# Kernel optimization log

Measured on AMD Instinct MI355X. Metric: run time of the kernel, lower is better.

The kernel has to match this reference:

```python
import jax, jax.numpy as jnp
import numpy as np

N_ANCHORS = 10647
N_CLASSES = 80
N_OUT = 5 + N_CLASSES
N_GT = 2048
POS_IOU = 0.7
NEG_IOU = 0.3
N_SAMPLE = 256
POS_RATIO = 0.5


def _cxcy_to_corners(b):
    return jnp.concatenate([b[:, :2] - b[:, 2:4] / 2, b[:, :2] + b[:, 2:4] / 2], axis=-1)


def _iou(a, b):
    # a: [N,4] corner boxes, b: [M,4] corner boxes -> [N,M]
    lt = jnp.maximum(a[:, None, :2], b[None, :, :2])
    rb = jnp.minimum(a[:, None, 2:], b[None, :, 2:])
    wh = jnp.clip(rb - lt, 0.0)
    inter = wh[..., 0] * wh[..., 1]
    area_a = (a[:, 2] - a[:, 0]) * (a[:, 3] - a[:, 1])
    area_b = (b[:, 2] - b[:, 0]) * (b[:, 3] - b[:, 1])
    return inter / (area_a[:, None] + area_b[None, :] - inter)


def _bce_logits(x, t):
    # numerically stable BCEWithLogits, elementwise
    return jnp.maximum(x, 0.0) - x * t + jnp.log1p(jnp.exp(-jnp.abs(x)))


def _demote_first(labels, value, excess):
    # demote the first `excess` anchors (in index order) whose label == value to -1,
    # mirroring torch's nonzero()[randperm(excess)] which always hits the first
    # `excess` entries of the nonzero list
    m = labels == value
    cum = jnp.cumsum(m.astype(jnp.int32))
    return jnp.where(m & (cum <= excess), -1.0, labels)


def _generate_targets(priors, gt_boxes, gt_labels):
    ious = _iou(_cxcy_to_corners(priors[:, :4]), _cxcy_to_corners(gt_boxes))  # [N, M]
    gt_max_index = jnp.argmax(ious, axis=0)       # [M] best anchor per gt
    anchor_max_ious = jnp.max(ious, axis=1)       # [N]
    anchor_max_index = jnp.argmax(ious, axis=1)   # [N]
    labels = jnp.full((N_ANCHORS,), -1.0, dtype=ious.dtype)
    labels = labels.at[gt_max_index].set(1.0)
    labels = jnp.where(anchor_max_ious >= POS_IOU, 1.0, labels)
    labels = jnp.where(anchor_max_ious < NEG_IOU, 0.0, labels)
    n_pos_quota = int(POS_RATIO * N_SAMPLE)
    n_pos_actual = jnp.sum(labels == 1.0)
    labels = _demote_first(labels, 1.0, jnp.maximum(n_pos_actual - n_pos_quota, 0))
    n_neg_req = N_SAMPLE - jnp.sum(labels == 1.0)
    n_neg_actual = jnp.sum(labels == 0.0)
    labels = _demote_first(labels, 0.0, jnp.maximum(n_neg_actual - n_neg_req, 0))
    anchor_gt_box = gt_boxes[anchor_max_index]    # [N,4] matched gt box per anchor
    anchor_cls = gt_labels[anchor_max_index] + 5  # [N] one-hot class column per anchor
    targets = jnp.zeros((N_ANCHORS, N_OUT), dtype=gt_boxes.dtype)
    targets = targets.at[:, :4].set(anchor_gt_box)
    targets = targets.at[:, 4].set(labels)
    targets = targets.at[jnp.arange(N_ANCHORS), anchor_cls].set(1.0)
    return targets


def _forward(predictions, gt_boxes, gt_labels, priors):
    targets = _generate_targets(priors, gt_boxes, gt_labels)
    pred = predictions[0]                          # [N, N_OUT]
    labels = targets[:, 4]
    pos = (labels == 1.0).astype(pred.dtype)
    neg = (labels == 0.0).astype(pred.dtype)
    n_pos = jnp.maximum(jnp.sum(pos), 1.0)
    n_neg = jnp.maximum(jnp.sum(neg), 1.0)
    # masked-mean MSE over x,y,w,h on positive anchors
    diff2 = (pred[:, :4] - targets[:, :4]) ** 2
    loss_box = jnp.sum(pos[:, None] * diff2, axis=0) / n_pos
    loss_conf_obj = jnp.sum(pos * _bce_logits(pred[:, 4], targets[:, 4])) / n_pos
    loss_conf_nonobj = jnp.sum(neg * _bce_logits(pred[:, 4], targets[:, 4])) / n_neg
    loss_class = jnp.sum(pos[:, None] * _bce_logits(pred[:, 5:], targets[:, 5:])) / (n_pos * N_CLASSES)
    total_loss = jnp.sum(loss_box) + loss_conf_obj + loss_conf_nonobj + loss_class
    return pred, total_loss


def setup_inputs() -> dict:
    key = jax.random.key(0)
    k1, k2, k3, k4 = jax.random.split(key, 4)
    predictions = jax.random.normal(k1, (1, N_ANCHORS, N_OUT), dtype=jnp.float32)
    gt_boxes = jax.random.uniform(k2, (N_GT, 4), dtype=jnp.float32, minval=0.05, maxval=0.95)
    gt_labels = jax.random.randint(k3, (N_GT,), 0, N_CLASSES)
    priors = jax.random.uniform(k4, (N_ANCHORS, N_OUT), dtype=jnp.float32, minval=0.05, maxval=0.95)
    return {"predictions": predictions, "gt_boxes": gt_boxes, "gt_labels": gt_labels, "priors": priors}


def reference(predictions, gt_boxes, gt_labels, priors):
    return _forward(predictions, gt_boxes, gt_labels, priors)
```

## Files before the change

kernel.cpp:

```cpp
#include <hip/hip_runtime.h>
#include <math.h>

#define N_ANCH 10647
#define NA_PAD 10688
#define N_GT   2048
#define N_OUTC 85
#define PRED_ELEMS (N_ANCH * N_OUTC)
#define PRED_V4    (PRED_ELEMS / 4)
#define N_CHUNK    42

#define ABX 21
#define ABY 32
#define NBLK_A (ABX * ABY)
#define GBX 4
#define GBY 167
#define NBLK_G (GBX * GBY)
#define NBLK_IOU (NBLK_A + NBLK_G)
#define CPY_PER_BLK ((PRED_V4 + NBLK_IOU - 1) / NBLK_IOU)

struct WS {
    float4 ac[NA_PAD];
    float4 gc[N_GT];
    unsigned long long akey[N_ANCH];
    unsigned long long gkey[N_GT];
    float aa[NA_PAD];
    float ga[N_GT];
    int cnt_p[N_CHUNK], cnt_n[N_CHUNK];
    unsigned int sync;
};

__device__ __forceinline__ float bce(float x, float t) {
    return fmaxf(x, 0.0f) - x * t + log1pf(expf(-fabsf(x)));
}

__device__ __forceinline__ unsigned long long packkey(float iou, int idx) {
    return ((unsigned long long)__float_as_uint(iou) << 32) |
           (unsigned)(~(unsigned)idx);
}

__global__ __launch_bounds__(256) void k_prep(const float* __restrict__ gtb,
                                              const float* __restrict__ priors,
                                              WS* __restrict__ ws) {
    int i = blockIdx.x * 256 + threadIdx.x;
    if (i < NA_PAD) {
        float4 c = make_float4(0.f, 0.f, 0.f, 0.f);
        float ar = 0.f;
        if (i < N_ANCH) {
            float cx = priors[i*N_OUTC+0], cy = priors[i*N_OUTC+1];
            float w  = priors[i*N_OUTC+2], h  = priors[i*N_OUTC+3];
            c = make_float4(cx - w*0.5f, cy - h*0.5f, cx + w*0.5f, cy + h*0.5f);
            ar = (c.z - c.x) * (c.w - c.y);
            ws->akey[i] = 0ull;
        }
        ws->ac[i] = c;
        ws->aa[i] = ar;
    }
    if (i < N_GT) {
        float4 v = ((const float4*)gtb)[i];
        float4 c = make_float4(v.x - v.z*0.5f, v.y - v.w*0.5f,
                               v.x + v.z*0.5f, v.y + v.w*0.5f);
        ws->gc[i] = c;
        ws->ga[i] = (c.z - c.x) * (c.w - c.y);
        ws->gkey[i] = 0ull;
    }
    if (i == 0) ws->sync = 0u;
}

__global__ __launch_bounds__(256) void k_iou(const float* __restrict__ pred,
                                             float* __restrict__ out,
                                             WS* __restrict__ ws) {
    int b = blockIdx.x, t = threadIdx.x;
    if (t < CPY_PER_BLK) {
        int idx = b * CPY_PER_BLK + t;
        if (idx < PRED_V4)
            ((float4*)out)[idx] = ((const float4*)pred)[idx];
    }
    if (b == 0 && t == 0) {
        out[PRED_ELEMS - 3] = pred[PRED_ELEMS - 3];
        out[PRED_ELEMS - 2] = pred[PRED_ELEMS - 2];
        out[PRED_ELEMS - 1] = pred[PRED_ELEMS - 1];
        out[PRED_ELEMS] = 0.0f;
    }

    if (b < NBLK_A) {
        int bx = b % ABX, by = b / ABX;
        int jbase = by * 64;
        int i0 = bx * 512 + t, i1 = i0 + 256;
        bool v0 = (i0 < N_ANCH), v1 = (i1 < N_ANCH);
        int ri0 = v0 ? i0 : 0, ri1 = v1 ? i1 : 0;
        float4 a0 = ws->ac[ri0]; float aa0 = ws->aa[ri0];
        float4 a1 = ws->ac[ri1]; float aa1 = ws->aa[ri1];
        float I0 = -1.f, S0 = 1.f, I1 = -1.f, S1 = 1.f;
        int bj0 = 0, bj1 = 0;
#pragma unroll 4
        for (int jj = 0; jj < 64; ++jj) {
            float4 g = ws->gc[jbase + jj];
            float ga = ws->ga[jbase + jj];
            float lx = fmaxf(a0.x, g.x), ly = fmaxf(a0.y, g.y);
            float rx = fminf(a0.z, g.z), ry = fminf(a0.w, g.w);
            float In = fmaxf(rx - lx, 0.f) * fmaxf(ry - ly, 0.f);
            float Sn = aa0 + ga;
            bool c = In * S0 > I0 * Sn;
            I0 = c ? In : I0; S0 = c ? Sn : S0; bj0 = c ? jj : bj0;
            lx = fmaxf(a1.x, g.x); ly = fmaxf(a1.y, g.y);
            rx = fminf(a1.z, g.z); ry = fminf(a1.w, g.w);
            In = fmaxf(rx - lx, 0.f) * fmaxf(ry - ly, 0.f);
            Sn = aa1 + ga;
            c = In * S1 > I1 * Sn;
            I1 = c ? In : I1; S1 = c ? Sn : S1; bj1 = c ? jj : bj1;
        }
        if (v0) atomicMax(&ws->akey[i0], packkey(I0 / (S0 - I0), jbase + bj0));
        if (v1) atomicMax(&ws->akey[i1], packkey(I1 / (S1 - I1), jbase + bj1));
    } else {
        int b2 = b - NBLK_A;
        int bx = b2 % GBX, by = b2 / GBX;
        int ibase = by * 64;
        int j0 = bx * 512 + t, j1 = j0 + 256;
        float4 g0 = ws->gc[j0]; float ga0 = ws->ga[j0];
        float4 g1 = ws->gc[j1]; float ga1 = ws->ga[j1];
        float I0 = -1.f, S0 = 1.f, I1 = -1.f, S1 = 1.f;
        int bi0 = 0, bi1 = 0;
#pragma unroll 4
        for (int ii = 0; ii < 64; ++ii) {
            float4 a = ws->ac[ibase + ii];
            float aa = ws->aa[ibase + ii];
            float lx = fmaxf(a.x, g0.x), ly = fmaxf(a.y, g0.y);
            float rx = fminf(a.z, g0.z), ry = fminf(a.w, g0.w);
            float In = fmaxf(rx - lx, 0.f) * fmaxf(ry - ly, 0.f);
            float Sn = aa + ga0;
            bool c = In * S0 > I0 * Sn;
            I0 = c ? In : I0; S0 = c ? Sn : S0; bi0 = c ? ii : bi0;
            lx = fmaxf(a.x, g1.x); ly = fmaxf(a.y, g1.y);
            rx = fminf(a.z, g1.z); ry = fminf(a.w, g1.w);
            In = fmaxf(rx - lx, 0.f) * fmaxf(ry - ly, 0.f);
            Sn = aa + ga1;
            c = In * S1 > I1 * Sn;
            I1 = c ? In : I1; S1 = c ? Sn : S1; bi1 = c ? ii : bi1;
        }
        atomicMax(&ws->gkey[j0], packkey(I0 / (S0 - I0), ibase + bi0));
        atomicMax(&ws->gkey[j1], packkey(I1 / (S1 - I1), ibase + bi1));
    }
}

__global__ __launch_bounds__(256) void k_tail2(const float* __restrict__ pred,
                                               const float* __restrict__ gtb,
                                               const int* __restrict__ gtl,
                                               WS* __restrict__ ws,
                                               float* __restrict__ out) {
    __shared__ int sFlg[256];
    __shared__ int wA[4], wB[4];
    __shared__ int wps[4], wns[4];
    __shared__ int sCp[N_CHUNK], sCn[N_CHUNK];
    __shared__ int    sPosI[256];
    __shared__ float4 sPosBox[256];
    __shared__ int    sPosCls[256];
    __shared__ int    sNegI[256];
    __shared__ float  red[12];
    int b = blockIdx.x, t = threadIdx.x, lane = t & 63, wid = t >> 6;
    int base = b * 256;

    sFlg[t] = 0;
    __syncthreads();
    for (int j = t; j < N_GT; j += 256) {
        int ai = (int)(~(unsigned)(ws->gkey[j]));
        int rel = ai - base;
        if ((unsigned)rel < 256u) sFlg[rel] = 1;
    }
    __syncthreads();
    int i = base + t;
    int lab = -2;
    if (i < N_ANCH) {
        float amax = __uint_as_float((unsigned)(ws->akey[i] >> 32));
        lab = (amax < 0.3f) ? 0 : ((amax >= 0.7f || sFlg[t]) ? 1 : -1);
    }
    bool f1 = (lab == 1), f0 = (lab == 0);
    unsigned long long b1 = __ballot(f1), b0v = __ballot(f0);
    if (lane == 0) { wA[wid] = __popcll(b1); wB[wid] = __popcll(b0v); }
    __syncthreads();
    if (t == 0) {
        int cp = wA[0] + wA[1] + wA[2] + wA[3];
        int cn = wB[0] + wB[1] + wB[2] + wB[3];
        __hip_atomic_store(&ws->cnt_p[b], cp, __ATOMIC_RELAXED, __HIP_MEMORY_SCOPE_AGENT);
        __hip_atomic_store(&ws->cnt_n[b], cn, __ATOMIC_RELAXED, __HIP_MEMORY_SCOPE_AGENT);
        __hip_atomic_fetch_add(&ws->sync, 1u, __ATOMIC_RELEASE, __HIP_MEMORY_SCOPE_AGENT);
        while (__hip_atomic_load(&ws->sync, __ATOMIC_ACQUIRE, __HIP_MEMORY_SCOPE_AGENT)
               < (unsigned)N_CHUNK)
            __builtin_amdgcn_s_sleep(2);
    }
    __syncthreads();
    if (t < N_CHUNK) {
        sCp[t] = __hip_atomic_load(&ws->cnt_p[t], __ATOMIC_ACQUIRE, __HIP_MEMORY_SCOPE_AGENT);
        sCn[t] = __hip_atomic_load(&ws->cnt_n[t], __ATOMIC_ACQUIRE, __HIP_MEMORY_SCOPE_AGENT);
    }
    __syncthreads();
    int npa = 0, nna = 0, pb = 0, nb = 0;
#pragma unroll
    for (int c = 0; c < N_CHUNK; ++c) {
        int cp = sCp[c], cn = sCn[c];
        if (c < b) { pb += cp; nb += cn; }
        npa += cp; nna += cn;
    }
    int excess_pos = (npa > 128) ? (npa - 128) : 0;
    int n_pos_f = npa - excess_pos;
    int n_neg_req = 256 - n_pos_f;
    int excess_neg = (nna > n_neg_req) ? (nna - n_neg_req) : 0;
    int n_neg_f = nna - excess_neg;

    unsigned long long pm = (2ull << lane) - 1ull;
    int r1 = __popcll(b1 & pm), r0 = __popcll(b0v & pm);
    if (lane == 0) { wps[wid] = __popcll(b1); wns[wid] = __popcll(b0v); }
    __syncthreads();
    int p1 = 0, p0 = 0, cpB = 0, cnB = 0;
    for (int w = 0; w < 4; ++w) {
        int v1 = wps[w], v0 = wns[w];
        cpB += v1; cnB += v0;
        if (w < wid) { p1 += v1; p0 += v0; }
    }
    int thp = excess_pos - pb; thp = (thp < 0) ? 0 : thp;
    int thn = excess_neg - nb; thn = (thn < 0) ? 0 : thn;
    if (f1) {
        int L = p1 + r1;
        if (L > thp) {
            int slot = L - thp - 1;
            sPosI[slot] = i;
            unsigned am = ~(unsigned)(ws->akey[i]);
            sPosBox[slot] = ((const float4*)gtb)[am];
            sPosCls[slot] = gtl[am] + 5;
        }
    }
    if (f0) {
        int L = p0 + r0;
        if (L > thn) sNegI[L - thn - 1] = i;
    }
    __syncthreads();
    int nP = cpB - thp; nP = (nP < 0) ? 0 : nP;
    int nN = cnB - thn; nN = (nN < 0) ? 0 : nN;

    float acc_a = 0.f, acc_c = 0.f, acc_n = 0.f;
    int nT = nP * N_OUTC;
    for (int u = t; u < nT; u += 256) {
        int pi = u / N_OUTC, col = u - pi * N_OUTC;
        float p = pred[sPosI[pi] * N_OUTC + col];
        if (col < 4) {
            float d = p - ((const float*)&sPosBox[pi])[col];
            acc_a += d * d;
        } else if (col == 4) {
            acc_a += bce(p, 1.0f);
        } else {
            acc_c += bce(p, (col == sPosCls[pi]) ? 1.0f : 0.0f);
        }
    }
    for (int u = t; u < nN; u += 256)
        acc_n += bce(pred[sNegI[u] * N_OUTC + 4], 0.0f);

    for (int o = 32; o; o >>= 1) {
        acc_a += __shfl_down(acc_a, o);
        acc_c += __shfl_down(acc_c, o);
        acc_n += __shfl_down(acc_n, o);
    }
    if (lane == 0) { red[wid] = acc_a; red[4 + wid] = acc_c; red[8 + wid] = acc_n; }
    __syncthreads();
    if (t == 0) {
        float A  = red[0] + red[1] + red[2]  + red[3];
        float C  = red[4] + red[5] + red[6]  + red[7];
        float Nn = red[8] + red[9] + red[10] + red[11];
        float np = fmaxf((float)n_pos_f, 1.0f);
        float nn = fmaxf((float)n_neg_f, 1.0f);
        float contrib = A / np + Nn / nn + C / (np * 80.0f);
        if (contrib != 0.0f) atomicAdd(&out[PRED_ELEMS], contrib);
    }
}

extern "C" void kernel_launch(void* const* d_in, const int* in_sizes, int n_in,
                              void* d_out, int out_size, void* d_ws, size_t ws_size,
                              hipStream_t stream) {
    const float* pred   = (const float*)d_in[0];
    const float* gtb    = (const float*)d_in[1];
    const int*   gtl    = (const int*)d_in[2];
    const float* priors = (const float*)d_in[3];
    float* out = (float*)d_out;
    WS* ws = (WS*)d_ws;

    k_prep<<<dim3(N_CHUNK), 256, 0, stream>>>(gtb, priors, ws);
    k_iou<<<dim3(NBLK_IOU), 256, 0, stream>>>(pred, out, ws);
    k_tail2<<<dim3(N_CHUNK), 256, 0, stream>>>(pred, gtb, gtl, ws, out);
}
```

Measured before the change: 65.98 us.

## Fuse prep, IoU and tail kernels into one persistent kernel with grid barriers

```diff
diff --git a/kernel.cpp b/kernel.cpp
--- a/kernel.cpp
+++ b/kernel.cpp
@@ -11,14 +11,17 @@
 
 #define ABX 21
 #define ABY 32
-#define NBLK_A (ABX * ABY)
+#define NTILE_A (ABX * ABY)
 #define GBX 4
 #define GBY 167
-#define NBLK_G (GBX * GBY)
-#define NBLK_IOU (NBLK_A + NBLK_G)
-#define CPY_PER_BLK ((PRED_V4 + NBLK_IOU - 1) / NBLK_IOU)
+#define NTILE (NTILE_A + GBX * GBY)
+#define NBLK 512
+#define NTHREADS (NBLK * 256)
 
 struct WS {
+    unsigned int sync_b1; unsigned int pad1[31];
+    unsigned int sync_b2; unsigned int pad2[31];
+    unsigned int sync_t;  unsigned int pad3[31];
     float4 ac[NA_PAD];
     float4 gc[N_GT];
     unsigned long long akey[N_ANCH];
@@ -26,8 +29,8 @@
     float aa[NA_PAD];
     float ga[N_GT];
     int cnt_p[N_CHUNK], cnt_n[N_CHUNK];
-    unsigned int sync;
 };
+#define MEMSET_BYTES 384
 
 __device__ __forceinline__ float bce(float x, float t) {
     return fmaxf(x, 0.0f) - x * t + log1pf(expf(-fabsf(x)));
@@ -38,115 +41,12 @@
            (unsigned)(~(unsigned)idx);
 }
 
-__global__ __launch_bounds__(256) void k_prep(const float* __restrict__ gtb,
-                                              const float* __restrict__ priors,
-                                              WS* __restrict__ ws) {
-    int i = blockIdx.x * 256 + threadIdx.x;
-    if (i < NA_PAD) {
-        float4 c = make_float4(0.f, 0.f, 0.f, 0.f);
-        float ar = 0.f;
-        if (i < N_ANCH) {
-            float cx = priors[i*N_OUTC+0], cy = priors[i*N_OUTC+1];
-            float w  = priors[i*N_OUTC+2], h  = priors[i*N_OUTC+3];
-            c = make_float4(cx - w*0.5f, cy - h*0.5f, cx + w*0.5f, cy + h*0.5f);
-            ar = (c.z - c.x) * (c.w - c.y);
-            ws->akey[i] = 0ull;
-        }
-        ws->ac[i] = c;
-        ws->aa[i] = ar;
-    }
-    if (i < N_GT) {
-        float4 v = ((const float4*)gtb)[i];
-        float4 c = make_float4(v.x - v.z*0.5f, v.y - v.w*0.5f,
-                               v.x + v.z*0.5f, v.y + v.w*0.5f);
-        ws->gc[i] = c;
-        ws->ga[i] = (c.z - c.x) * (c.w - c.y);
-        ws->gkey[i] = 0ull;
-    }
-    if (i == 0) ws->sync = 0u;
-}
-
-__global__ __launch_bounds__(256) void k_iou(const float* __restrict__ pred,
-                                             float* __restrict__ out,
-                                             WS* __restrict__ ws) {
-    int b = blockIdx.x, t = threadIdx.x;
-    if (t < CPY_PER_BLK) {
-        int idx = b * CPY_PER_BLK + t;
-        if (idx < PRED_V4)
-            ((float4*)out)[idx] = ((const float4*)pred)[idx];
-    }
-    if (b == 0 && t == 0) {
-        out[PRED_ELEMS - 3] = pred[PRED_ELEMS - 3];
-        out[PRED_ELEMS - 2] = pred[PRED_ELEMS - 2];
-        out[PRED_ELEMS - 1] = pred[PRED_ELEMS - 1];
-        out[PRED_ELEMS] = 0.0f;
-    }
-
-    if (b < NBLK_A) {
-        int bx = b % ABX, by = b / ABX;
-        int jbase = by * 64;
-        int i0 = bx * 512 + t, i1 = i0 + 256;
-        bool v0 = (i0 < N_ANCH), v1 = (i1 < N_ANCH);
-        int ri0 = v0 ? i0 : 0, ri1 = v1 ? i1 : 0;
-        float4 a0 = ws->ac[ri0]; float aa0 = ws->aa[ri0];
-        float4 a1 = ws->ac[ri1]; float aa1 = ws->aa[ri1];
-        float I0 = -1.f, S0 = 1.f, I1 = -1.f, S1 = 1.f;
-        int bj0 = 0, bj1 = 0;
-#pragma unroll 4
-        for (int jj = 0; jj < 64; ++jj) {
-            float4 g = ws->gc[jbase + jj];
-            float ga = ws->ga[jbase + jj];
-            float lx = fmaxf(a0.x, g.x), ly = fmaxf(a0.y, g.y);
-            float rx = fminf(a0.z, g.z), ry = fminf(a0.w, g.w);
-            float In = fmaxf(rx - lx, 0.f) * fmaxf(ry - ly, 0.f);
-            float Sn = aa0 + ga;
-            bool c = In * S0 > I0 * Sn;
-            I0 = c ? In : I0; S0 = c ? Sn : S0; bj0 = c ? jj : bj0;
-            lx = fmaxf(a1.x, g.x); ly = fmaxf(a1.y, g.y);
-            rx = fminf(a1.z, g.z); ry = fminf(a1.w, g.w);
-            In = fmaxf(rx - lx, 0.f) * fmaxf(ry - ly, 0.f);
-            Sn = aa1 + ga;
-            c = In * S1 > I1 * Sn;
-            I1 = c ? In : I1; S1 = c ? Sn : S1; bj1 = c ? jj : bj1;
-        }
-        if (v0) atomicMax(&ws->akey[i0], packkey(I0 / (S0 - I0), jbase + bj0));
-        if (v1) atomicMax(&ws->akey[i1], packkey(I1 / (S1 - I1), jbase + bj1));
-    } else {
-        int b2 = b - NBLK_A;
-        int bx = b2 % GBX, by = b2 / GBX;
-        int ibase = by * 64;
-        int j0 = bx * 512 + t, j1 = j0 + 256;
-        float4 g0 = ws->gc[j0]; float ga0 = ws->ga[j0];
-        float4 g1 = ws->gc[j1]; float ga1 = ws->ga[j1];
-        float I0 = -1.f, S0 = 1.f, I1 = -1.f, S1 = 1.f;
-        int bi0 = 0, bi1 = 0;
-#pragma unroll 4
-        for (int ii = 0; ii < 64; ++ii) {
-            float4 a = ws->ac[ibase + ii];
-            float aa = ws->aa[ibase + ii];
-            float lx = fmaxf(a.x, g0.x), ly = fmaxf(a.y, g0.y);
-            float rx = fminf(a.z, g0.z), ry = fminf(a.w, g0.w);
-            float In = fmaxf(rx - lx, 0.f) * fmaxf(ry - ly, 0.f);
-            float Sn = aa + ga0;
-            bool c = In * S0 > I0 * Sn;
-            I0 = c ? In : I0; S0 = c ? Sn : S0; bi0 = c ? ii : bi0;
-            lx = fmaxf(a.x, g1.x); ly = fmaxf(a.y, g1.y);
-            rx = fminf(a.z, g1.z); ry = fminf(a.w, g1.w);
-            In = fmaxf(rx - lx, 0.f) * fmaxf(ry - ly, 0.f);
-            Sn = aa + ga1;
-            c = In * S1 > I1 * Sn;
-            I1 = c ? In : I1; S1 = c ? Sn : S1; bi1 = c ? ii : bi1;
-        }
-        atomicMax(&ws->gkey[j0], packkey(I0 / (S0 - I0), ibase + bi0));
-        atomicMax(&ws->gkey[j1], packkey(I1 / (S1 - I1), ibase + bi1));
-    }
-}
-
-__global__ __launch_bounds__(256) void k_tail2(const float* __restrict__ pred,
+__global__ __launch_bounds__(256) void k_fused(const float* __restrict__ pred,
                                                const float* __restrict__ gtb,
                                                const int* __restrict__ gtl,
-                                               WS* __restrict__ ws,
-                                               float* __restrict__ out) {
+                                               const float* __restrict__ priors,
+                                               float* __restrict__ out,
+                                               WS* __restrict__ ws) {
     __shared__ int sFlg[256];
     __shared__ int wA[4], wB[4];
     __shared__ int wps[4], wns[4];
@@ -156,9 +56,123 @@
     __shared__ int    sPosCls[256];
     __shared__ int    sNegI[256];
     __shared__ float  red[12];
+
     int b = blockIdx.x, t = threadIdx.x, lane = t & 63, wid = t >> 6;
+    int gtid = b * 256 + t;
+
+    for (int idx = gtid; idx < PRED_V4; idx += NTHREADS)
+        ((float4*)out)[idx] = ((const float4*)pred)[idx];
+    if (gtid == 0) {
+        out[PRED_ELEMS - 3] = pred[PRED_ELEMS - 3];
+        out[PRED_ELEMS - 2] = pred[PRED_ELEMS - 2];
+        out[PRED_ELEMS - 1] = pred[PRED_ELEMS - 1];
+        out[PRED_ELEMS] = 0.0f;
+    }
+    if (gtid < NA_PAD) {
+        float4 c = make_float4(0.f, 0.f, 0.f, 0.f);
+        float ar = 0.f;
+        if (gtid < N_ANCH) {
+            float cx = priors[gtid*N_OUTC+0], cy = priors[gtid*N_OUTC+1];
+            float w  = priors[gtid*N_OUTC+2], h  = priors[gtid*N_OUTC+3];
+            c = make_float4(cx - w*0.5f, cy - h*0.5f, cx + w*0.5f, cy + h*0.5f);
+            ar = (c.z - c.x) * (c.w - c.y);
+            ws->akey[gtid] = 0ull;
+        }
+        ws->ac[gtid] = c;
+        ws->aa[gtid] = ar;
+    }
+    if (gtid < N_GT) {
+        float4 v = ((const float4*)gtb)[gtid];
+        float4 c = make_float4(v.x - v.z*0.5f, v.y - v.w*0.5f,
+                               v.x + v.z*0.5f, v.y + v.w*0.5f);
+        ws->gc[gtid] = c;
+        ws->ga[gtid] = (c.z - c.x) * (c.w - c.y);
+        ws->gkey[gtid] = 0ull;
+    }
+
+    __syncthreads();
+    if (t == 0) {
+        __hip_atomic_fetch_add(&ws->sync_b1, 1u, __ATOMIC_RELEASE, __HIP_MEMORY_SCOPE_AGENT);
+        while (__hip_atomic_load(&ws->sync_b1, __ATOMIC_ACQUIRE, __HIP_MEMORY_SCOPE_AGENT)
+               < (unsigned)NBLK)
+            __builtin_amdgcn_s_sleep(2);
+    }
+    __syncthreads();
+
+    for (int vb = b; vb < NTILE; vb += NBLK) {
+        if (vb < NTILE_A) {
+            int bx = vb % ABX, by = vb / ABX;
+            int jbase = by * 64;
+            int i0 = bx * 512 + t, i1 = i0 + 256;
+            bool v0 = (i0 < N_ANCH), v1 = (i1 < N_ANCH);
+            int ri0 = v0 ? i0 : 0, ri1 = v1 ? i1 : 0;
+            float4 a0 = ws->ac[ri0]; float aa0 = ws->aa[ri0];
+            float4 a1 = ws->ac[ri1]; float aa1 = ws->aa[ri1];
+            float I0 = -1.f, S0 = 1.f, I1 = -1.f, S1 = 1.f;
+            int bj0 = 0, bj1 = 0;
+#pragma unroll 4
+            for (int jj = 0; jj < 64; ++jj) {
+                float4 g = ws->gc[jbase + jj];
+                float ga = ws->ga[jbase + jj];
+                float lx = fmaxf(a0.x, g.x), ly = fmaxf(a0.y, g.y);
+                float rx = fminf(a0.z, g.z), ry = fminf(a0.w, g.w);
+                float In = fmaxf(rx - lx, 0.f) * fmaxf(ry - ly, 0.f);
+                float Sn = aa0 + ga;
+                bool c = In * S0 > I0 * Sn;
+                I0 = c ? In : I0; S0 = c ? Sn : S0; bj0 = c ? jj : bj0;
+                lx = fmaxf(a1.x, g.x); ly = fmaxf(a1.y, g.y);
+                rx = fminf(a1.z, g.z); ry = fminf(a1.w, g.w);
+                In = fmaxf(rx - lx, 0.f) * fmaxf(ry - ly, 0.f);
+                Sn = aa1 + ga;
+                c = In * S1 > I1 * Sn;
+                I1 = c ? In : I1; S1 = c ? Sn : S1; bj1 = c ? jj : bj1;
+            }
+            if (v0) atomicMax(&ws->akey[i0], packkey(I0 / (S0 - I0), jbase + bj0));
+            if (v1) atomicMax(&ws->akey[i1], packkey(I1 / (S1 - I1), jbase + bj1));
+        } else {
+            int b2 = vb - NTILE_A;
+            int bx = b2 % GBX, by = b2 / GBX;
+            int ibase = by * 64;
+            int j0 = bx * 512 + t, j1 = j0 + 256;
+            float4 g0 = ws->gc[j0]; float ga0 = ws->ga[j0];
+            float4 g1 = ws->gc[j1]; float ga1 = ws->ga[j1];
+            float I0 = -1.f, S0 = 1.f, I1 = -1.f, S1 = 1.f;
+            int bi0 = 0, bi1 = 0;
+#pragma unroll 4
+            for (int ii = 0; ii < 64; ++ii) {
+                float4 a = ws->ac[ibase + ii];
+                float aa = ws->aa[ibase + ii];
+                float lx = fmaxf(a.x, g0.x), ly = fmaxf(a.y, g0.y);
+                float rx = fminf(a.z, g0.z), ry = fminf(a.w, g0.w);
+                float In = fmaxf(rx - lx, 0.f) * fmaxf(ry - ly, 0.f);
+                float Sn = aa + ga0;
+                bool c = In * S0 > I0 * Sn;
+                I0 = c ? In : I0; S0 = c ? Sn : S0; bi0 = c ? ii : bi0;
+                lx = fmaxf(a.x, g1.x); ly = fmaxf(a.y, g1.y);
+                rx = fminf(a.z, g1.z); ry = fminf(a.w, g1.w);
+                In = fmaxf(rx - lx, 0.f) * fmaxf(ry - ly, 0.f);
+                Sn = aa + ga1;
+                c = In * S1 > I1 * Sn;
+                I1 = c ? In : I1; S1 = c ? Sn : S1; bi1 = c ? ii : bi1;
+            }
+            atomicMax(&ws->gkey[j0], packkey(I0 / (S0 - I0), ibase + bi0));
+            atomicMax(&ws->gkey[j1], packkey(I1 / (S1 - I1), ibase + bi1));
+        }
+    }
+
+    __syncthreads();
+    if (t == 0) {
+        __hip_atomic_fetch_add(&ws->sync_b2, 1u, __ATOMIC_RELEASE, __HIP_MEMORY_SCOPE_AGENT);
+    }
+    if (b >= N_CHUNK) return;
+    if (t == 0) {
+        while (__hip_atomic_load(&ws->sync_b2, __ATOMIC_ACQUIRE, __HIP_MEMORY_SCOPE_AGENT)
+               < (unsigned)NBLK)
+            __builtin_amdgcn_s_sleep(2);
+    }
+    __syncthreads();
+
     int base = b * 256;
-
     sFlg[t] = 0;
     __syncthreads();
     for (int j = t; j < N_GT; j += 256) {
@@ -174,16 +188,16 @@
         lab = (amax < 0.3f) ? 0 : ((amax >= 0.7f || sFlg[t]) ? 1 : -1);
     }
     bool f1 = (lab == 1), f0 = (lab == 0);
-    unsigned long long b1 = __ballot(f1), b0v = __ballot(f0);
-    if (lane == 0) { wA[wid] = __popcll(b1); wB[wid] = __popcll(b0v); }
+    unsigned long long b1m = __ballot(f1), b0v = __ballot(f0);
+    if (lane == 0) { wA[wid] = __popcll(b1m); wB[wid] = __popcll(b0v); }
     __syncthreads();
     if (t == 0) {
         int cp = wA[0] + wA[1] + wA[2] + wA[3];
         int cn = wB[0] + wB[1] + wB[2] + wB[3];
         __hip_atomic_store(&ws->cnt_p[b], cp, __ATOMIC_RELAXED, __HIP_MEMORY_SCOPE_AGENT);
         __hip_atomic_store(&ws->cnt_n[b], cn, __ATOMIC_RELAXED, __HIP_MEMORY_SCOPE_AGENT);
-        __hip_atomic_fetch_add(&ws->sync, 1u, __ATOMIC_RELEASE, __HIP_MEMORY_SCOPE_AGENT);
-        while (__hip_atomic_load(&ws->sync, __ATOMIC_ACQUIRE, __HIP_MEMORY_SCOPE_AGENT)
+        __hip_atomic_fetch_add(&ws->sync_t, 1u, __ATOMIC_RELEASE, __HIP_MEMORY_SCOPE_AGENT);
+        while (__hip_atomic_load(&ws->sync_t, __ATOMIC_ACQUIRE, __HIP_MEMORY_SCOPE_AGENT)
                < (unsigned)N_CHUNK)
             __builtin_amdgcn_s_sleep(2);
     }
@@ -207,8 +221,8 @@
     int n_neg_f = nna - excess_neg;
 
     unsigned long long pm = (2ull << lane) - 1ull;
-    int r1 = __popcll(b1 & pm), r0 = __popcll(b0v & pm);
-    if (lane == 0) { wps[wid] = __popcll(b1); wns[wid] = __popcll(b0v); }
+    int r1 = __popcll(b1m & pm), r0 = __popcll(b0v & pm);
+    if (lane == 0) { wps[wid] = __popcll(b1m); wns[wid] = __popcll(b0v); }
     __syncthreads();
     int p1 = 0, p0 = 0, cpB = 0, cnB = 0;
     for (int w = 0; w < 4; ++w) {
@@ -281,7 +295,6 @@
     float* out = (float*)d_out;
     WS* ws = (WS*)d_ws;
 
-    k_prep<<<dim3(N_CHUNK), 256, 0, stream>>>(gtb, priors, ws);
-    k_iou<<<dim3(NBLK_IOU), 256, 0, stream>>>(pred, out, ws);
-    k_tail2<<<dim3(N_CHUNK), 256, 0, stream>>>(pred, gtb, gtl, ws, out);
+    hipMemsetAsync(d_ws, 0, MEMSET_BYTES, stream);
+    k_fused<<<dim3(NBLK), 256, 0, stream>>>(pred, gtb, gtl, priors, out, ws);
 }
```

Result: slower. 143.7 us (+117.8%).
